# Optimization experiments

Measured on AMD Instinct MI355X. Metric: run time of the kernel, lower is better.

## Reference

```python
import jax, jax.numpy as jnp
from jax import lax
import numpy as np

N, R, WM, HM = 512, 64, 6, 6        # batch, n_rooms, padded room width/height
E, MX, MY = 16, 32, 24              # embedding width, map dims (from source)
MAP_CH = [32, 64, 64]; KS = [5, 3, 3]
ROOM_CH = [64, 64]; OUT = 64


def _boundaries(m):
    # faithful translation of _compute_room_boundaries (numpy, static room data)
    left = np.zeros_like(m); left[0] = m[0]; left[1:] = np.clip(m[1:] - m[:-1], 0, None)
    right = np.zeros_like(m); right[-1] = m[-1]; right[:-1] = np.clip(m[:-1] - m[1:], 0, None)
    up = np.zeros_like(m); up[:, 0] = m[:, 0]; up[:, 1:] = np.clip(m[:, 1:] - m[:, :-1], 0, None)
    down = np.zeros_like(m); down[:, -1] = m[:, -1]; down[:, :-1] = np.clip(m[:, :-1] - m[:, 1:], 0, None)
    return np.stack([left, right, up, down], 0)


def _make_rooms(rng):
    # synthetic Crateria-like rooms: [R, 9, WM, HM] = map, 4 door masks, 4 boundaries
    rooms = np.zeros((R, 9, WM, HM), np.float32)
    for i in range(R):
        w = int(rng.integers(2, WM + 1)); h = int(rng.integers(2, HM + 1))
        m = np.zeros((WM, HM), np.float32); m[:w, :h] = 1.0
        doors = (rng.random((4, WM, HM)) < 0.2).astype(np.float32) * m
        rooms[i] = np.concatenate([m[None], doors, _boundaries(m)], 0)
    return rooms


def setup_inputs():
    rng = np.random.default_rng(0)
    rooms = jnp.asarray(_make_rooms(rng))
    key = jax.random.key(0)
    ks = jax.random.split(key, 16)
    px = jax.random.randint(ks[0], (N, R, 1), 0, MX - WM + 1)
    py = jax.random.randint(ks[1], (N, R, 1), 0, MY - HM + 1)
    room_positions = jnp.concatenate([px, py], -1).astype(jnp.int32)
    emb = jax.random.normal(ks[2], (R, E), jnp.float32)
    cw = [10 + E] + MAP_CH
    inp = {"room_positions": room_positions, "rooms": rooms, "emb": emb}
    for i, k in enumerate(KS):
        inp[f"w{i}"] = jax.random.normal(ks[3 + i], (cw[i + 1], cw[i], k, k), jnp.float32) / np.float32(np.sqrt(cw[i] * k * k))
        inp[f"b{i}"] = jnp.zeros((cw[i + 1],), jnp.float32)
    rc = [MAP_CH[-1]] + ROOM_CH + [OUT]
    for i in range(3):
        inp[f"rw{i}"] = jax.random.normal(ks[8 + i], (rc[i + 1], rc[i]), jnp.float32) / np.float32(np.sqrt(rc[i]))
        inp[f"rb{i}"] = jnp.zeros((rc[i + 1],), jnp.float32)
    return inp


def _forward(room_positions, rooms, emb, w0, b0, w1, b1, w2, b2, rw0, rb0, rw1, rb1, rw2, rb2):
    n = room_positions.shape[0]
    # linearized scatter/gather indices for all rooms at once: [n, R*WM*HM]
    idx_x = room_positions[:, :, 0:1] + jnp.arange(WM)  # [n,R,WM]
    idx_y = room_positions[:, :, 1:2] + jnp.arange(HM)  # [n,R,HM]
    lin = (idx_x[:, :, :, None] * MY + idx_y[:, :, None, :]).reshape(n, R * WM * HM)
    vals9 = rooms.transpose(1, 0, 2, 3).reshape(9, R * WM * HM)
    valsE = (emb.T[:, :, None, None] * rooms[:, 0][None]).reshape(E, R * WM * HM)

    def scat(lin_i):
        fm = jnp.zeros((9, MX * MY), rooms.dtype).at[:, lin_i].add(vals9)
        em = jnp.zeros((E, MX * MY), rooms.dtype).at[:, lin_i].add(valsE)
        return fm, em

    fm, em = jax.vmap(scat)(lin)
    bg = jnp.ones((n, 1, MX * MY), rooms.dtype)  # channel 9 = 1.0 background
    X = jnp.concatenate([fm, bg, em], 1).reshape(n, 10 + E, MX, MY)
    # SAME-padded Conv2d + ReLU stack
    for w, b, k in ((w0, b0, KS[0]), (w1, b1, KS[1]), (w2, b2, KS[2])):
        p = k // 2
        X = lax.conv_general_dilated(X, w, (1, 1), [(p, p), (p, p)],
                                     dimension_numbers=("NCHW", "OIHW", "NCHW"))
        X = jax.nn.relu(X + b[None, :, None, None])
    # decode_map: gather each room's patch, mask by room map, sum spatially -> [n,C,R]
    C = X.shape[1]
    Xf = X.reshape(n, C, MX * MY)
    g = jax.vmap(lambda xi, li: xi[:, li])(Xf, lin).reshape(n, C, R, WM, HM)
    Y = (g * rooms[:, 0][None, None]).sum((3, 4))
    # 1x1 Conv1d head (pointwise over channels)
    Y = jax.nn.relu(jnp.einsum("oc,ncr->nor", rw0, Y) + rb0[None, :, None])
    Y = jax.nn.relu(jnp.einsum("oc,ncr->nor", rw1, Y) + rb1[None, :, None])
    Y = jnp.einsum("oc,ncr->nor", rw2, Y) + rb2[None, :, None]
    return Y.transpose(0, 2, 1)  # [n, R, output_width]


def reference(room_positions, rooms, emb, w0, b0, w1, b1, w2, b2, rw0, rb0, rw1, rb1, rw2, rb2):
    return _forward(room_positions, rooms, emb, w0, b0, w1, b1, w2, b2,
                    rw0, rb0, rw1, rb1, rw2, rb2)
```

## Files before the change

kernel.cpp:

```cpp
#include <hip/hip_runtime.h>
#include <hip/hip_bf16.h>
#include <stdint.h>

typedef short v8s __attribute__((ext_vector_type(8)));
typedef float v4f __attribute__((ext_vector_type(4)));

#define TPB 1024

#define X0_OFF 0
#define X1_OFF 106496
#define X2_OFF 0
#define X3_OFF 106496
#define YA_OFF 0
#define YB_OFF 16384
#define EMB_OFF 57344
#define MK_OFF 159744
#define CH8_OFF 160256
#define RPL_OFF 162560
#define MW_OFF 163072
#define SMEM_BYTES 163520

#define WS0_U 0
#define WS1_U 3200
#define WS2_U 5504
#define WS_UNITS 10112

#define SWZ64(row) ((((row) >> 1) & 3) << 4)

__device__ __forceinline__ uint16_t f2b(float f) {
    __hip_bfloat16 h = __float2bfloat16(f);
    return *reinterpret_cast<uint16_t*>(&h);
}
__device__ __forceinline__ uint32_t pkbf(float lo, float hi) {
    return (uint32_t)f2b(lo) | ((uint32_t)f2b(hi) << 16);
}
__device__ __forceinline__ float b2f(uint16_t h) {
    return __uint_as_float(((uint32_t)h) << 16);
}

__global__ void prep_weights(const float* __restrict__ w0,
                             const float* __restrict__ w1,
                             const float* __restrict__ w2,
                             uint8_t* __restrict__ ws)
{
    int u = blockIdx.x * 256 + threadIdx.x;
    if (u >= WS_UNITS) return;
    int l = u & 63, fid = u >> 6;
    const float* src; int IC, KS_, t, kf, m;
    if (fid < 50)      { src = w0; IC = 26; KS_ = 5; t = fid >> 1; kf = 0; m = fid & 1; }
    else if (fid < 86) { int v = fid - 50; src = w1; IC = 32; KS_ = 3; t = v >> 2; kf = 0; m = v & 3; }
    else               { int v = fid - 86; src = w2; IC = 64; KS_ = 3; t = v >> 3; kf = (v >> 2) & 1; m = v & 3; }
    int oc = m * 16 + (l & 15);
    int kb = kf * 32 + ((l >> 4) * 8);
    int ky = t / KS_, kx = t - ky * KS_;
    v8s out;
#pragma unroll
    for (int j = 0; j < 8; ++j) {
        int k = kb + j;
        float v = (k < IC) ? src[((oc * IC + k) * KS_ + ky) * KS_ + kx] : 0.f;
        out[j] = (short)f2b(v);
    }
    ((v8s*)ws)[u] = out;
}

template<int MT, int KF, int TAPS, int KS, int PAD,
         int IN_OFF, int IN_SH, int IN_ROWS, int WS_BASE, int MT_TOT>
__device__ __forceinline__ void conv_core(const uint8_t* smem, const v8s* __restrict__ wsv,
                                          int l, const int* px, const int* py,
                                          v4f (&acc)[MT][3])
{
    const int kgoff = ((l >> 4) << 4);
    for (int t = 0; t < TAPS; ++t) {
        const int ky = t / KS, kx = t - ky * KS;
        const int dx = ky - PAD, dy = kx - PAD;
        v8s af[MT][KF];
#pragma unroll
        for (int m = 0; m < MT; ++m)
#pragma unroll
            for (int kf = 0; kf < KF; ++kf)
                af[m][kf] = wsv[WS_BASE + ((t * KF + kf) * MT_TOT + m) * 64 + l];
#pragma unroll
        for (int i = 0; i < 3; ++i) {
            const int xi = px[i] + dx;
            const int rowp = xi * IN_ROWS + py[i] + dy + PAD;
            int a;
            if (IN_SH == 7) a = ((rowp << 7) | kgoff) ^ ((rowp & 7) << 4);
            else            a = ((rowp << 6) | kgoff) ^ SWZ64(rowp);
            a = ((unsigned)xi < 32u) ? a : kgoff;
            a += IN_OFF;
            const v8s bf0 = *(const v8s*)(smem + a);
#pragma unroll
            for (int m = 0; m < MT; ++m)
                acc[m][i] = __builtin_amdgcn_mfma_f32_16x16x32_bf16(af[m][0], bf0, acc[m][i], 0, 0, 0);
            if (KF == 2) {
                const v8s bf1 = *(const v8s*)(smem + (a ^ 64));
#pragma unroll
                for (int m = 0; m < MT; ++m)
                    acc[m][i] = __builtin_amdgcn_mfma_f32_16x16x32_bf16(af[m][1], bf1, acc[m][i], 0, 0, 0);
            }
        }
    }
}

template<int MTOT, int M0, int M1, int OUT_OFF, int OUT_SH, int OUT_ROWS, int OUT_PAD>
__device__ __forceinline__ void conv_epi(uint8_t* smem, const float* __restrict__ bias,
                                         v4f (&acc)[MTOT][3], const int* px, const int* py, int kg)
{
#pragma unroll
    for (int m = M0; m < M1; ++m) {
        const float* bp = bias + m * 16 + kg * 4;
        const float bb0 = bp[0], bb1 = bp[1], bb2 = bp[2], bb3 = bp[3];
#pragma unroll
        for (int i = 0; i < 3; ++i) {
            const float v0 = fmaxf(acc[m][i][0] + bb0, 0.f);
            const float v1 = fmaxf(acc[m][i][1] + bb1, 0.f);
            const float v2 = fmaxf(acc[m][i][2] + bb2, 0.f);
            const float v3 = fmaxf(acc[m][i][3] + bb3, 0.f);
            uint2 pk;
            pk.x = pkbf(v0, v1);
            pk.y = pkbf(v2, v3);
            const int rowp = px[i] * OUT_ROWS + py[i] + OUT_PAD;
            const int coff = (m - M0) * 32 + (kg << 3);
            int a;
            if (OUT_SH == 7) a = ((rowp << 7) | coff) ^ ((rowp & 7) << 4);
            else             a = ((rowp << 6) | coff) ^ SWZ64(rowp);
            *(uint2*)(smem + OUT_OFF + a) = pk;
        }
    }
}

__device__ __forceinline__ void gather_half(const uint8_t* smem,
                                            const uint32_t* __restrict__ mk,
                                            const int* __restrict__ rpl,
                                            int gr, int gl, float* yreg)
{
    const int pxr = rpl[gr * 2], pyr = rpl[gr * 2 + 1];
    const uint32_t mlo = mk[gr * 2], mhi = mk[gr * 2 + 1];
    float s0=0,s1=0,s2=0,s3=0,s4=0,s5=0,s6=0,s7=0;
#pragma unroll
    for (int cell = 0; cell < 36; ++cell) {
        const uint32_t w = (cell < 32) ? mlo : mhi;
        if ((w >> (cell & 31)) & 1u) {
            const int p = (pxr + cell / 6) * 24 + pyr + (cell % 6);
            const v8s v = *(const v8s*)(smem + X3_OFF +
                (((p << 6) | (gl << 4)) ^ SWZ64(p)));
            s0 += b2f((uint16_t)v[0]);
            s1 += b2f((uint16_t)v[1]);
            s2 += b2f((uint16_t)v[2]);
            s3 += b2f((uint16_t)v[3]);
            s4 += b2f((uint16_t)v[4]);
            s5 += b2f((uint16_t)v[5]);
            s6 += b2f((uint16_t)v[6]);
            s7 += b2f((uint16_t)v[7]);
        }
    }
    yreg[0]=s0; yreg[1]=s1; yreg[2]=s2; yreg[3]=s3;
    yreg[4]=s4; yreg[5]=s5; yreg[6]=s6; yreg[7]=s7;
}

template<bool RELU>
__device__ __forceinline__ void mlp_layer(uint8_t* smem, int inoff, int outoff,
                                          const float* __restrict__ W,
                                          const float* __restrict__ bias, int tid)
{
    const int og = tid >> 6, r = tid & 63;
    const int ogs = __builtin_amdgcn_readfirstlane(og);
    const int swz = (r & 7) << 4;
    float acc[4];
#pragma unroll
    for (int oo = 0; oo < 4; ++oo) acc[oo] = bias[ogs * 4 + oo];
    const float* Wb = W + ogs * 4 * 64;
#pragma unroll
    for (int cg = 0; cg < 16; ++cg) {
        const v4f v = *(const v4f*)(smem + inoff + ((r * 256 + cg * 16) ^ swz));
#pragma unroll
        for (int oo = 0; oo < 4; ++oo) {
            const float* wr = Wb + oo * 64 + cg * 4;
            acc[oo] = fmaf(wr[0], v[0], acc[oo]);
            acc[oo] = fmaf(wr[1], v[1], acc[oo]);
            acc[oo] = fmaf(wr[2], v[2], acc[oo]);
            acc[oo] = fmaf(wr[3], v[3], acc[oo]);
        }
    }
    if (RELU)
#pragma unroll
        for (int oo = 0; oo < 4; ++oo) acc[oo] = fmaxf(acc[oo], 0.f);
    const v4f o0 = {acc[0], acc[1], acc[2], acc[3]};
    *(v4f*)(smem + outoff + ((r * 256 + ogs * 16) ^ swz)) = o0;
}

__global__ __launch_bounds__(TPB)
void fused_main(const int* __restrict__ rpos,
                const float* __restrict__ rooms,
                const float* __restrict__ emb,
                const float* __restrict__ b0, const float* __restrict__ b1,
                const float* __restrict__ b2,
                const float* __restrict__ rw0, const float* __restrict__ rb0,
                const float* __restrict__ rw1, const float* __restrict__ rb1,
                const float* __restrict__ rw2, const float* __restrict__ rb2,
                const uint8_t* __restrict__ ws,
                float* __restrict__ out)
{
    __shared__ __align__(16) uint8_t smem[SMEM_BYTES];
    const int tid = threadIdx.x, n = blockIdx.x;
    const int* rp = rpos + n * 128;
    const v8s* wsv = (const v8s*)ws;
    uint32_t* mk  = (uint32_t*)(smem + MK_OFF);
    uint8_t*  ch8 = smem + CH8_OFF;
    int*      rpl = (int*)(smem + RPL_OFF);
    uint32_t* mw  = (uint32_t*)(smem + MW_OFF);
    float*    embl = (float*)(smem + EMB_OFF);

    embl[tid] = emb[tid];
    if (tid < 112) mw[tid] = 0;
    if (tid >= 128 && tid < 256) mk[tid - 128] = 0;
    if (tid >= 256 && tid < 384) rpl[tid - 256] = rp[tid - 256];
    __syncthreads();
    if (tid < 64) {
        const int pxr = rpl[2 * tid], pyr = rpl[2 * tid + 1];
        const uint32_t bit = 1u << (tid & 31);
        const int xb = (tid >> 5) * 32, yb = 64 + (tid >> 5) * 24;
#pragma unroll
        for (int i = 0; i < 6; ++i) atomicOr(&mw[xb + pxr + i], bit);
#pragma unroll
        for (int j = 0; j < 6; ++j) atomicOr(&mw[yb + pyr + j], bit);
    }
    for (int q = tid; q < 2304; q += TPB) {
        const int r = (q * 1821) >> 16;
        const int cell = q - r * 36;
        const float* base = rooms + r * 324 + cell;
        uint32_t bits = 0;
#pragma unroll
        for (int c = 1; c < 9; ++c)
            bits |= (base[c * 36] != 0.f ? 1u : 0u) << (c - 1);
        ch8[q] = (uint8_t)bits;
        if (base[0] != 0.f) atomicOr(&mk[r * 2 + (cell >> 5)], 1u << (cell & 31));
    }
    __syncthreads();

    if (tid < 768) {
        const int x = (tid * 2731) >> 16;
        const int y = tid - x * 24;
        float a[26];
#pragma unroll
        for (int c = 0; c < 26; ++c) a[c] = 0.f;
        a[9] = 1.f;
        uint32_t mlo = mw[x] & mw[64 + y];
        uint32_t mhi = mw[32 + x] & mw[88 + y];
#pragma unroll 1
        for (int half = 0; half < 2; ++half) {
            uint32_t mm = half ? mhi : mlo;
            const int rb = half ? 32 : 0;
            while (mm) {
                const int r = rb + __builtin_ctz(mm);
                mm &= mm - 1;
                const int cell = (x - rpl[2 * r]) * 6 + (y - rpl[2 * r + 1]);
                const uint32_t w = mk[r * 2 + (cell >> 5)];
                if ((w >> (cell & 31)) & 1u) {
                    a[0] += 1.f;
                    const uint32_t bits = ch8[r * 36 + cell];
#pragma unroll
                    for (int c = 0; c < 8; ++c)
                        a[1 + c] += (float)((bits >> c) & 1u);
                    const float* er = embl + r * 16;
#pragma unroll
                    for (int e = 0; e < 16; ++e) a[10 + e] += er[e];
                }
            }
        }
        const int row = x * 28 + y + 2;
        const int swz = SWZ64(row);
#pragma unroll
        for (int cg = 0; cg < 4; ++cg) {
            float c[8];
#pragma unroll
            for (int j = 0; j < 8; ++j) {
                const int ci = cg * 8 + j;
                c[j] = (ci < 26) ? a[(ci < 26) ? ci : 0] : 0.f;
            }
            uint2 p0, p1;
            p0.x = pkbf(c[0], c[1]); p0.y = pkbf(c[2], c[3]);
            p1.x = pkbf(c[4], c[5]); p1.y = pkbf(c[6], c[7]);
            const int a0 = X0_OFF + (((row << 6) | (cg << 4)) ^ swz);
            *(uint2*)(smem + a0)     = p0;
            *(uint2*)(smem + a0 + 8) = p1;
        }
    } else {
        const int base = (tid - 768) * 2;
#pragma unroll
        for (int k = 0; k < 2; ++k) {
            const int u = base + k;
            const int rowi = u >> 2, slot = u & 3;
            const int x = rowi >> 2, yp = rowi & 3;
            const int row = x * 28 + ((yp < 2) ? yp : yp + 24);
            *(v8s*)(smem + X0_OFF + (((row << 6) | (slot << 4)) ^ SWZ64(row))) =
                (v8s){0,0,0,0,0,0,0,0};
        }
    }
    __syncthreads();

    const int l = tid & 63, wv = tid >> 6, kg = l >> 4;
    int px[3], py[3];
#pragma unroll
    for (int i = 0; i < 3; ++i) {
        const int p = (wv + 16 * i) * 16 + (l & 15);
        const int x = (p * 2731) >> 16;
        px[i] = x; py[i] = p - x * 24;
    }

    {
        if (tid < 256) {
            const int rowi = tid >> 2, slot = tid & 3;
            const int x = rowi >> 1;
            const int rowp = x * 26 + ((rowi & 1) ? 25 : 0);
            *(v8s*)(smem + X1_OFF + (((rowp << 6) | (slot << 4)) ^ SWZ64(rowp))) =
                (v8s){0,0,0,0,0,0,0,0};
        }
        v4f acc[2][3];
#pragma unroll
        for (int m = 0; m < 2; ++m)
#pragma unroll
            for (int i = 0; i < 3; ++i) acc[m][i] = (v4f){0.f,0.f,0.f,0.f};
        conv_core<2,1,25,5,2, X0_OFF,6,28, WS0_U,2>(smem, wsv, l, px, py, acc);
        conv_epi<2,0,2, X1_OFF,6,26,1>(smem, b0, acc, px, py, kg);
    }
    __syncthreads();

    {
        if (tid < 512) {
            const int rowi = tid >> 3, slot = tid & 7;
            const int x = rowi >> 1;
            const int rowp = x * 26 + ((rowi & 1) ? 25 : 0);
            *(v8s*)(smem + X2_OFF + (((rowp << 7) | (slot << 4)) ^ ((rowp & 7) << 4))) =
                (v8s){0,0,0,0,0,0,0,0};
        }
        v4f acc[4][3];
#pragma unroll
        for (int m = 0; m < 4; ++m)
#pragma unroll
            for (int i = 0; i < 3; ++i) acc[m][i] = (v4f){0.f,0.f,0.f,0.f};
        conv_core<4,1,9,3,1, X1_OFF,6,26, WS1_U,4>(smem, wsv, l, px, py, acc);
        conv_epi<4,0,4, X2_OFF,7,26,1>(smem, b1, acc, px, py, kg);
    }
    __syncthreads();

    float yregA[8], yregB[8];
    {
        v4f acc[4][3];
#pragma unroll
        for (int m = 0; m < 4; ++m)
#pragma unroll
            for (int i = 0; i < 3; ++i) acc[m][i] = (v4f){0.f,0.f,0.f,0.f};
        conv_core<4,2,9,3,1, X2_OFF,7,26, WS2_U,4>(smem, wsv, l, px, py, acc);
        conv_epi<4,0,2, X3_OFF,6,24,0>(smem, b2, acc, px, py, kg);
        __syncthreads();
        if (tid < 256) gather_half(smem, mk, rpl, tid >> 2, tid & 3, yregA);
        __syncthreads();
        conv_epi<4,2,4, X3_OFF,6,24,0>(smem, b2, acc, px, py, kg);
        __syncthreads();
        if (tid < 256) gather_half(smem, mk, rpl, tid >> 2, tid & 3, yregB);
        __syncthreads();
    }

    if (tid < 256) {
        const int gr = tid >> 2, gl = tid & 3;
        const int swz = (gr & 7) << 4;
        const int baseA = gr * 256 + gl * 32;
        const int baseB = baseA + 128;
        *(v4f*)(smem + YA_OFF + (baseA ^ swz))        = (v4f){yregA[0], yregA[1], yregA[2], yregA[3]};
        *(v4f*)(smem + YA_OFF + ((baseA + 16) ^ swz)) = (v4f){yregA[4], yregA[5], yregA[6], yregA[7]};
        *(v4f*)(smem + YA_OFF + (baseB ^ swz))        = (v4f){yregB[0], yregB[1], yregB[2], yregB[3]};
        *(v4f*)(smem + YA_OFF + ((baseB + 16) ^ swz)) = (v4f){yregB[4], yregB[5], yregB[6], yregB[7]};
    }
    __syncthreads();

    mlp_layer<true >(smem, YA_OFF, YB_OFF, rw0, rb0, tid);
    __syncthreads();
    mlp_layer<true >(smem, YB_OFF, YA_OFF, rw1, rb1, tid);
    __syncthreads();
    mlp_layer<false>(smem, YA_OFF, YB_OFF, rw2, rb2, tid);
    __syncthreads();

    {
        const int r = tid >> 4, cg = tid & 15;
        const int swz = (r & 7) << 4;
        const v4f v = *(const v4f*)(smem + YB_OFF + ((r * 256 + cg * 16) ^ swz));
        *(v4f*)(out + n * 4096 + r * 64 + cg * 4) = v;
    }
}

extern "C" void kernel_launch(void* const* d_in, const int* in_sizes, int n_in,
                              void* d_out, int out_size, void* d_ws, size_t ws_size,
                              hipStream_t stream) {
    const int*   rpos  = (const int*)  d_in[0];
    const float* rooms = (const float*)d_in[1];
    const float* emb   = (const float*)d_in[2];
    const float* w0    = (const float*)d_in[3];
    const float* b0    = (const float*)d_in[4];
    const float* w1    = (const float*)d_in[5];
    const float* b1    = (const float*)d_in[6];
    const float* w2    = (const float*)d_in[7];
    const float* b2    = (const float*)d_in[8];
    const float* rw0   = (const float*)d_in[9];
    const float* rb0   = (const float*)d_in[10];
    const float* rw1   = (const float*)d_in[11];
    const float* rb1   = (const float*)d_in[12];
    const float* rw2   = (const float*)d_in[13];
    const float* rb2   = (const float*)d_in[14];
    float* out = (float*)d_out;
    uint8_t* ws = (uint8_t*)d_ws;

    const int n = in_sizes[0] / 128;
    hipLaunchKernelGGL(prep_weights, dim3((WS_UNITS + 255) / 256), dim3(256), 0, stream,
                       w0, w1, w2, ws);
    hipLaunchKernelGGL(fused_main, dim3(n), dim3(TPB), 0, stream,
                       rpos, rooms, emb, b0, b1, b2,
                       rw0, rb0, rw1, rb1, rw2, rb2, ws, out);
}
```

Before: 109.1 us.

## Precompute room masks in prep kernel and gather both channel halves at once

Room-map bitmasks and door/boundary bit bytes are now computed once by the prep kernel into the workspace, instead of being rebuilt from global rooms data in every block. The main kernel just copies them into shared memory. The last conv layer writes its two channel halves into separate shared buffers, so a single 512-thread gather pass replaces two 256-thread passes and removes two barriers. This relies on the shared regions X3B, YA and YB not overlapping live data, which requires careful offset reuse.

```diff
diff --git a/kernel.cpp b/kernel.cpp
--- a/kernel.cpp
+++ b/kernel.cpp
@@ -10,9 +10,10 @@
 #define X0_OFF 0
 #define X1_OFF 106496
 #define X2_OFF 0
-#define X3_OFF 106496
-#define YA_OFF 0
-#define YB_OFF 16384
+#define X3A_OFF 106496
+#define X3B_OFF 0
+#define YA_OFF 49152
+#define YB_OFF 65536
 #define EMB_OFF 57344
 #define MK_OFF 159744
 #define CH8_OFF 160256
@@ -24,6 +25,9 @@
 #define WS1_U 3200
 #define WS2_U 5504
 #define WS_UNITS 10112
+#define WS_W_BYTES (WS_UNITS * 16)
+#define MKG_OFF  WS_W_BYTES
+#define CH8G_OFF (WS_W_BYTES + 512)
 
 #define SWZ64(row) ((((row) >> 1) & 3) << 4)
 
@@ -38,29 +42,53 @@
     return __uint_as_float(((uint32_t)h) << 16);
 }
 
-__global__ void prep_weights(const float* __restrict__ w0,
-                             const float* __restrict__ w1,
-                             const float* __restrict__ w2,
-                             uint8_t* __restrict__ ws)
+__global__ void prep_all(const float* __restrict__ w0,
+                         const float* __restrict__ w1,
+                         const float* __restrict__ w2,
+                         const float* __restrict__ rooms,
+                         uint8_t* __restrict__ ws)
 {
-    int u = blockIdx.x * 256 + threadIdx.x;
-    if (u >= WS_UNITS) return;
-    int l = u & 63, fid = u >> 6;
-    const float* src; int IC, KS_, t, kf, m;
-    if (fid < 50)      { src = w0; IC = 26; KS_ = 5; t = fid >> 1; kf = 0; m = fid & 1; }
-    else if (fid < 86) { int v = fid - 50; src = w1; IC = 32; KS_ = 3; t = v >> 2; kf = 0; m = v & 3; }
-    else               { int v = fid - 86; src = w2; IC = 64; KS_ = 3; t = v >> 3; kf = (v >> 2) & 1; m = v & 3; }
-    int oc = m * 16 + (l & 15);
-    int kb = kf * 32 + ((l >> 4) * 8);
-    int ky = t / KS_, kx = t - ky * KS_;
-    v8s out;
-#pragma unroll
-    for (int j = 0; j < 8; ++j) {
-        int k = kb + j;
-        float v = (k < IC) ? src[((oc * IC + k) * KS_ + ky) * KS_ + kx] : 0.f;
-        out[j] = (short)f2b(v);
-    }
-    ((v8s*)ws)[u] = out;
+    const int bid = blockIdx.x, t = threadIdx.x;
+    if (bid < 40) {
+        int u = bid * 256 + t;
+        if (u >= WS_UNITS) return;
+        int l = u & 63, fid = u >> 6;
+        const float* src; int IC, KS_, tt, kf, m;
+        if (fid < 50)      { src = w0; IC = 26; KS_ = 5; tt = fid >> 1; kf = 0; m = fid & 1; }
+        else if (fid < 86) { int v = fid - 50; src = w1; IC = 32; KS_ = 3; tt = v >> 2; kf = 0; m = v & 3; }
+        else               { int v = fid - 86; src = w2; IC = 64; KS_ = 3; tt = v >> 3; kf = (v >> 2) & 1; m = v & 3; }
+        int oc = m * 16 + (l & 15);
+        int kb = kf * 32 + ((l >> 4) * 8);
+        int ky = tt / KS_, kx = tt - ky * KS_;
+        v8s out;
+#pragma unroll
+        for (int j = 0; j < 8; ++j) {
+            int k = kb + j;
+            float v = (k < IC) ? src[((oc * IC + k) * KS_ + ky) * KS_ + kx] : 0.f;
+            out[j] = (short)f2b(v);
+        }
+        ((v8s*)ws)[u] = out;
+    } else if (bid < 49) {
+        const int q = (bid - 40) * 256 + t;
+        const int r = (q * 1821) >> 16;
+        const int cell = q - r * 36;
+        const float* base = rooms + r * 324 + cell;
+        uint32_t bits = 0;
+#pragma unroll
+        for (int c = 1; c < 9; ++c)
+            bits |= (base[c * 36] != 0.f ? 1u : 0u) << (c - 1);
+        ws[CH8G_OFF + q] = (uint8_t)bits;
+    } else {
+        if (t < 128) {
+            const int r = t >> 1, h = t & 1;
+            const float* rr = rooms + r * 324;
+            uint32_t m = 0;
+            const int c0 = h * 32, c1 = h ? 36 : 32;
+            for (int cell = c0; cell < c1; ++cell)
+                if (rr[cell] != 0.f) m |= 1u << (cell - c0);
+            ((uint32_t*)(ws + MKG_OFF))[t] = m;
+        }
+    }
 }
 
 template<int MT, int KF, int TAPS, int KS, int PAD,
@@ -127,35 +155,6 @@
             *(uint2*)(smem + OUT_OFF + a) = pk;
         }
     }
-}
-
-__device__ __forceinline__ void gather_half(const uint8_t* smem,
-                                            const uint32_t* __restrict__ mk,
-                                            const int* __restrict__ rpl,
-                                            int gr, int gl, float* yreg)
-{
-    const int pxr = rpl[gr * 2], pyr = rpl[gr * 2 + 1];
-    const uint32_t mlo = mk[gr * 2], mhi = mk[gr * 2 + 1];
-    float s0=0,s1=0,s2=0,s3=0,s4=0,s5=0,s6=0,s7=0;
-#pragma unroll
-    for (int cell = 0; cell < 36; ++cell) {
-        const uint32_t w = (cell < 32) ? mlo : mhi;
-        if ((w >> (cell & 31)) & 1u) {
-            const int p = (pxr + cell / 6) * 24 + pyr + (cell % 6);
-            const v8s v = *(const v8s*)(smem + X3_OFF +
-                (((p << 6) | (gl << 4)) ^ SWZ64(p)));
-            s0 += b2f((uint16_t)v[0]);
-            s1 += b2f((uint16_t)v[1]);
-            s2 += b2f((uint16_t)v[2]);
-            s3 += b2f((uint16_t)v[3]);
-            s4 += b2f((uint16_t)v[4]);
-            s5 += b2f((uint16_t)v[5]);
-            s6 += b2f((uint16_t)v[6]);
-            s7 += b2f((uint16_t)v[7]);
-        }
-    }
-    yreg[0]=s0; yreg[1]=s1; yreg[2]=s2; yreg[3]=s3;
-    yreg[4]=s4; yreg[5]=s5; yreg[6]=s6; yreg[7]=s7;
 }
 
 template<bool RELU>
@@ -213,8 +212,10 @@
 
     embl[tid] = emb[tid];
     if (tid < 112) mw[tid] = 0;
-    if (tid >= 128 && tid < 256) mk[tid - 128] = 0;
+    if (tid >= 128 && tid < 256) mk[tid - 128] = ((const uint32_t*)(ws + MKG_OFF))[tid - 128];
     if (tid >= 256 && tid < 384) rpl[tid - 256] = rp[tid - 256];
+    if (tid >= 384 && tid < 960) ((uint32_t*)ch8)[tid - 384] =
+        ((const uint32_t*)(ws + CH8G_OFF))[tid - 384];
     __syncthreads();
     if (tid < 64) {
         const int pxr = rpl[2 * tid], pyr = rpl[2 * tid + 1];
@@ -224,17 +225,6 @@
         for (int i = 0; i < 6; ++i) atomicOr(&mw[xb + pxr + i], bit);
 #pragma unroll
         for (int j = 0; j < 6; ++j) atomicOr(&mw[yb + pyr + j], bit);
-    }
-    for (int q = tid; q < 2304; q += TPB) {
-        const int r = (q * 1821) >> 16;
-        const int cell = q - r * 36;
-        const float* base = rooms + r * 324 + cell;
-        uint32_t bits = 0;
-#pragma unroll
-        for (int c = 1; c < 9; ++c)
-            bits |= (base[c * 36] != 0.f ? 1u : 0u) << (c - 1);
-        ch8[q] = (uint8_t)bits;
-        if (base[0] != 0.f) atomicOr(&mk[r * 2 + (cell >> 5)], 1u << (cell & 31));
     }
     __syncthreads();
 
@@ -344,7 +334,6 @@
     }
     __syncthreads();
 
-    float yregA[8], yregB[8];
     {
         v4f acc[4][3];
 #pragma unroll
@@ -352,25 +341,39 @@
 #pragma unroll
             for (int i = 0; i < 3; ++i) acc[m][i] = (v4f){0.f,0.f,0.f,0.f};
         conv_core<4,2,9,3,1, X2_OFF,7,26, WS2_U,4>(smem, wsv, l, px, py, acc);
-        conv_epi<4,0,2, X3_OFF,6,24,0>(smem, b2, acc, px, py, kg);
+        conv_epi<4,0,2, X3A_OFF,6,24,0>(smem, b2, acc, px, py, kg);
         __syncthreads();
-        if (tid < 256) gather_half(smem, mk, rpl, tid >> 2, tid & 3, yregA);
+        conv_epi<4,2,4, X3B_OFF,6,24,0>(smem, b2, acc, px, py, kg);
         __syncthreads();
-        conv_epi<4,2,4, X3_OFF,6,24,0>(smem, b2, acc, px, py, kg);
-        __syncthreads();
-        if (tid < 256) gather_half(smem, mk, rpl, tid >> 2, tid & 3, yregB);
-        __syncthreads();
-    }
-
-    if (tid < 256) {
-        const int gr = tid >> 2, gl = tid & 3;
+    }
+    if (tid < 512) {
+        const int gr = tid >> 3, gg = tid & 7;
+        const int gl = gg & 3;
+        const int roff = (gg < 4) ? X3A_OFF : X3B_OFF;
+        const int pxr = rpl[gr * 2], pyr = rpl[gr * 2 + 1];
+        const uint32_t mlo = mk[gr * 2], mhi = mk[gr * 2 + 1];
+        float s0=0,s1=0,s2=0,s3=0,s4=0,s5=0,s6=0,s7=0;
+#pragma unroll
+        for (int cell = 0; cell < 36; ++cell) {
+            const uint32_t w = (cell < 32) ? mlo : mhi;
+            if ((w >> (cell & 31)) & 1u) {
+                const int p = (pxr + cell / 6) * 24 + pyr + (cell % 6);
+                const v8s v = *(const v8s*)(smem + roff +
+                    (((p << 6) | (gl << 4)) ^ SWZ64(p)));
+                s0 += b2f((uint16_t)v[0]);
+                s1 += b2f((uint16_t)v[1]);
+                s2 += b2f((uint16_t)v[2]);
+                s3 += b2f((uint16_t)v[3]);
+                s4 += b2f((uint16_t)v[4]);
+                s5 += b2f((uint16_t)v[5]);
+                s6 += b2f((uint16_t)v[6]);
+                s7 += b2f((uint16_t)v[7]);
+            }
+        }
+        const int base = gr * 256 + gl * 32 + (gg >> 2) * 128;
         const int swz = (gr & 7) << 4;
-        const int baseA = gr * 256 + gl * 32;
-        const int baseB = baseA + 128;
-        *(v4f*)(smem + YA_OFF + (baseA ^ swz))        = (v4f){yregA[0], yregA[1], yregA[2], yregA[3]};
-        *(v4f*)(smem + YA_OFF + ((baseA + 16) ^ swz)) = (v4f){yregA[4], yregA[5], yregA[6], yregA[7]};
-        *(v4f*)(smem + YA_OFF + (baseB ^ swz))        = (v4f){yregB[0], yregB[1], yregB[2], yregB[3]};
-        *(v4f*)(smem + YA_OFF + ((baseB + 16) ^ swz)) = (v4f){yregB[4], yregB[5], yregB[6], yregB[7]};
+        *(v4f*)(smem + YA_OFF + (base ^ swz))        = (v4f){s0, s1, s2, s3};
+        *(v4f*)(smem + YA_OFF + ((base + 16) ^ swz)) = (v4f){s4, s5, s6, s7};
     }
     __syncthreads();
 
@@ -411,8 +414,8 @@
     uint8_t* ws = (uint8_t*)d_ws;
 
     const int n = in_sizes[0] / 128;
-    hipLaunchKernelGGL(prep_weights, dim3((WS_UNITS + 255) / 256), dim3(256), 0, stream,
-                       w0, w1, w2, ws);
+    hipLaunchKernelGGL(prep_all, dim3(50), dim3(256), 0, stream,
+                       w0, w1, w2, rooms, ws);
     hipLaunchKernelGGL(fused_main, dim3(n), dim3(TPB), 0, stream,
                        rpos, rooms, emb, b0, b1, b2,
                        rw0, rb0, rw1, rb1, rw2, rb2, ws, out);
```

After: 104.3 us. -4.5%, faster.
